# Kernel tuning notes

Measured on AMD Instinct MI355X. Metric: run time of the kernel, lower is better.

Reference implementation:

```python
import jax, jax.numpy as jnp
import numpy as np

WS = 8          # partition (window) size
HEADS = 8
DH = 32         # dim_head
DEPTH = 2
SCALE = DH ** -0.5
LN_EPS = 1e-5


def _rel_pos_index_dis(h, w):
    ch, cw = np.arange(h), np.arange(w)
    coords = np.stack(np.meshgrid(ch, cw, indexing='ij'))          # [2,h,w]
    cf = coords.reshape(2, -1)                                      # [2,n]
    rel = (cf[:, :, None] - cf[:, None, :]).transpose(1, 2, 0)      # [n,n,2]
    dis = (rel[:, :, 0].astype(np.float32) / h) ** 2 + (rel[:, :, 1].astype(np.float32) / w) ** 2
    rel = rel.copy()
    rel[:, :, 0] += h - 1
    rel[:, :, 1] += w - 1
    rel[:, :, 0] *= 2 * w - 1
    return rel.sum(-1), dis                                          # [n,n] int, [n,n] float


def _ln(x, g, b):
    m = x.mean(-1, keepdims=True)
    v = jnp.var(x, axis=-1, keepdims=True)
    return (x - m) * jax.lax.rsqrt(v + LN_EPS) * g + b


def setup_inputs() -> dict:
    key = jax.random.key(0)
    ks = jax.random.split(key, 16)
    D, INNER, MLP = 256, HEADS * DH, 1024
    TBL = (2 * WS - 1) * (2 * WS - 1)  # 225
    s = 0.02
    inp = {
        'x':        jax.random.normal(ks[0], (4, 256, 128, 128), jnp.float32),
        'W_patch':  jax.random.normal(ks[1], (256, D), jnp.float32) * s,
        'b_patch':  jnp.zeros((D,), jnp.float32),
        'ln1_g':    jnp.ones((DEPTH, D), jnp.float32),
        'ln1_b':    jnp.zeros((DEPTH, D), jnp.float32),
        'Wqkv':     jax.random.normal(ks[2], (DEPTH, D, 3 * INNER), jnp.float32) * s,
        'headsita': jnp.tile(jnp.arange(1, HEADS + 1, dtype=jnp.float32) * 0.1, (DEPTH, 1)),
        'bias_table': jax.random.normal(ks[3], (DEPTH, TBL, HEADS), jnp.float32) * s,
        'Wout':     jax.random.normal(ks[4], (DEPTH, INNER, D), jnp.float32) * s,
        'bout':     jnp.zeros((DEPTH, D), jnp.float32),
        'ln2_g':    jnp.ones((DEPTH, D), jnp.float32),
        'ln2_b':    jnp.zeros((DEPTH, D), jnp.float32),
        'W1':       jax.random.normal(ks[5], (DEPTH, D, MLP), jnp.float32) * s,
        'b1':       jnp.zeros((DEPTH, MLP), jnp.float32),
        'W2':       jax.random.normal(ks[6], (DEPTH, MLP, D), jnp.float32) * s,
        'b2':       jnp.zeros((DEPTH, D), jnp.float32),
    }
    return inp


def reference(x, W_patch, b_patch, ln1_g, ln1_b, Wqkv, headsita, bias_table,
              Wout, bout, ln2_g, ln2_b, W1, b1, W2, b2):
    B, C, H, W = x.shape
    n = WS * WS
    rpi_np, dis_np = _rel_pos_index_dis(WS, WS)
    rpi = jnp.asarray(rpi_np.reshape(-1))           # [n*n] int, static gather index
    dis = jnp.asarray(dis_np)                       # [n,n]

    # window partition: [B,C,H,W] -> [nW, n, C]
    t = x.transpose(0, 2, 3, 1)
    t = t.reshape(B, H // WS, WS, W // WS, WS, C).transpose(0, 1, 3, 2, 4, 5)
    t = t.reshape(-1, n, C)
    # patch embedding (patch_size=1)
    t = t @ W_patch + b_patch                        # [nW, n, D]

    attns = []
    for l in range(DEPTH):
        h = _ln(t, ln1_g[l], ln1_b[l])
        qkv = h @ Wqkv[l]                            # [nW, n, 3*inner]
        q, k, v = jnp.split(qkv, 3, axis=-1)
        def heads(a):
            return a.reshape(a.shape[0], n, HEADS, DH).transpose(0, 2, 1, 3)
        q, k, v = heads(q), heads(k), heads(v)       # [nW, H, n, dh]
        dots0 = jnp.einsum('bhid,bhjd->bhij', q, k) * SCALE
        # relative position bias gather: [n*n] -> [n,n,heads] -> [heads,n,n]
        bias = bias_table[l][rpi].reshape(n, n, HEADS).transpose(2, 0, 1)
        # learned per-head gaussian decay on spatial distance
        factor = 1.0 / (2.0 * headsita[l] ** 2 + 1e-10)          # [heads]
        pos = jnp.exp(-factor[:, None, None] * dis[None, :, :])  # [heads,n,n]
        dots = dots0 + bias[None] + 0.01 * pos[None]
        attn = jax.nn.softmax(dots, axis=-1)
        o = jnp.einsum('bhij,bhjd->bhid', attn, v)   # [nW, H, n, dh]
        o = o.transpose(0, 2, 1, 3).reshape(-1, n, HEADS * DH)
        ax = o @ Wout[l] + bout[l]
        attns.append(jax.nn.softmax(dots0, axis=-1))
        t = ax + t
        h2 = _ln(t, ln2_g[l], ln2_b[l])
        t = jax.nn.relu(h2 @ W1[l] + b1[l]) @ W2[l] + b2[l] + t

    # recover + window reverse: [nW, n, D] -> [B, D, H, W]
    D = t.shape[-1]
    out = t.reshape(B, H // WS, W // WS, WS, WS, D).transpose(0, 1, 3, 2, 4, 5)
    out = out.reshape(B, H, W, D).transpose(0, 3, 1, 2)
    return out, jnp.stack(attns)
```

## Files before the change

### kernel.cpp

```cpp
#include <hip/hip_runtime.h>
#include <hip/hip_bf16.h>
#include <cstddef>
#include <cstdint>


#define ROWS      65536
#define DMODEL    256
#define NWIN      1024
#define NHEADS    8
#define QKV_N     768
#define MLP_N     1024
#define SCALE_F   0.17677669529663687f
#define LN_EPS_F  1e-5f

typedef float f32x4 __attribute__((ext_vector_type(4)));
typedef __bf16 bf16x8 __attribute__((ext_vector_type(8)));

#define CP16(gp, lp)                                                          \
  __builtin_amdgcn_global_load_lds(                                           \
      (const __attribute__((address_space(1))) unsigned int*)(gp),            \
      (__attribute__((address_space(3))) unsigned int*)(lp), 16, 0, 0)

__device__ __forceinline__ float bf2f(ushort u) {
  return __uint_as_float(((unsigned)u) << 16);
}

__global__ __launch_bounds__(256) void gather_k(const float* __restrict__ x,
                                                __hip_bfloat16* __restrict__ Xg) {
  size_t idx = (size_t)blockIdx.x * 256 + threadIdx.x;
  int c   = (int)(idx & 255);
  int row = (int)(idx >> 8);
  int i   = row & 63;
  int wxy = row >> 6;
  int wx  = wxy & 15;
  int wy  = (wxy >> 4) & 15;
  int b   = wxy >> 8;
  int y   = wy * 8 + (i >> 3);
  int xx  = wx * 8 + (i & 7);
  Xg[idx] = __float2bfloat16(x[(((size_t)b * 256 + c) * 128 + y) * 128 + xx]);
}

__global__ __launch_bounds__(256) void unwindow_k(const float* __restrict__ t,
                                                  float* __restrict__ out) {
  size_t idx = (size_t)blockIdx.x * 256 + threadIdx.x;
  int xx = (int)(idx & 127);
  size_t r = idx >> 7;
  int y = (int)(r & 127); r >>= 7;
  int d = (int)(r & 255);
  int b = (int)(r >> 8);
  int row = ((b * 16 + (y >> 3)) * 16 + (xx >> 3)) * 64 + (y & 7) * 8 + (xx & 7);
  out[idx] = t[(size_t)row * DMODEL + d];
}

__global__ __launch_bounds__(256) void transpose_k(const float* __restrict__ src,
                                                   __hip_bfloat16* __restrict__ dst,
                                                   int K, int N) {
  __shared__ float tile[32][33];
  int tx = threadIdx.x, ty = threadIdx.y;
  int n0 = blockIdx.x * 32, k0 = blockIdx.y * 32;
#pragma unroll
  for (int i = 0; i < 4; ++i)
    tile[ty + i * 8][tx] = src[(size_t)(k0 + ty + i * 8) * N + n0 + tx];
  __syncthreads();
#pragma unroll
  for (int i = 0; i < 4; ++i)
    dst[(size_t)(n0 + ty + i * 8) * K + k0 + tx] =
        __float2bfloat16(tile[tx][ty + i * 8]);
}

__global__ __launch_bounds__(256) void ln_k(const float* __restrict__ X,
                                            __hip_bfloat16* __restrict__ Y,
                                            const float* __restrict__ g,
                                            const float* __restrict__ b) {
  const int row = blockIdx.x;
  const int tid = threadIdx.x;
  float x = X[(size_t)row * DMODEL + tid];
  float s = x, s2 = x * x;
#pragma unroll
  for (int off = 32; off > 0; off >>= 1) {
    s  += __shfl_down(s,  off);
    s2 += __shfl_down(s2, off);
  }
  __shared__ float ls[4], ls2[4];
  int wave = tid >> 6, lane = tid & 63;
  if (lane == 0) { ls[wave] = s; ls2[wave] = s2; }
  __syncthreads();
  if (tid == 0) {
    float ts  = ls[0] + ls[1] + ls[2] + ls[3];
    float ts2 = ls2[0] + ls2[1] + ls2[2] + ls2[3];
    float m   = ts * (1.0f / DMODEL);
    float var = ts2 * (1.0f / DMODEL) - m * m;
    ls[0]  = m;
    ls2[0] = rsqrtf(var + LN_EPS_F);
  }
  __syncthreads();
  float m = ls[0], rr = ls2[0];
  Y[(size_t)row * DMODEL + tid] = __float2bfloat16((x - m) * rr * g[tid] + b[tid]);
}

template <bool BIAS, bool RELU, bool RES, bool OBF16>
__global__ __launch_bounds__(256) void mm_k(const ushort* __restrict__ A,
                                            const ushort* __restrict__ BT,
                                            const float* __restrict__ bias,
                                            const float* __restrict__ res,
                                            void* __restrict__ Cout,
                                            int M, int N, int K) {
  __shared__ ushort As[4096];
  __shared__ ushort Bs[4096];
  const int tid = threadIdx.x;
  const int bm = blockIdx.y << 7, bn = blockIdx.x << 7;
  const ushort* Ap = A + (size_t)(bm + (tid >> 2)) * K + ((tid & 3) << 3);
  const ushort* Bp = BT + (size_t)(bn + (tid >> 2)) * K + ((tid & 3) << 3);
  const size_t k64 = (size_t)64 * K;
  const int lane = tid & 63, wave = tid >> 6;
  const int wm = (wave & 1) << 6, wn = (wave >> 1) << 6;
  const int lrow = lane & 15, kq = lane >> 4;
  const ushort* aF = &As[(wm + lrow) * 32 + kq * 8];
  const ushort* bF = &Bs[(wn + lrow) * 32 + kq * 8];
  f32x4 acc[4][4] = {};
  for (int k0 = 0; k0 < K; k0 += 32) {
    __syncthreads();
    CP16(Ap, &As[tid * 8]);
    CP16(Ap + k64, &As[2048 + tid * 8]);
    CP16(Bp, &Bs[tid * 8]);
    CP16(Bp + k64, &Bs[2048 + tid * 8]);
    Ap += 32; Bp += 32;
    __syncthreads();
    bf16x8 af[4], bf[4];
#pragma unroll
    for (int i = 0; i < 4; ++i) af[i] = *(const bf16x8*)(aF + i * 512);
#pragma unroll
    for (int j = 0; j < 4; ++j) bf[j] = *(const bf16x8*)(bF + j * 512);
#pragma unroll
    for (int i = 0; i < 4; ++i)
#pragma unroll
      for (int j = 0; j < 4; ++j)
        acc[i][j] =
            __builtin_amdgcn_mfma_f32_16x16x32_bf16(af[i], bf[j], acc[i][j], 0, 0, 0);
  }
  const int r0 = bm + wm + kq * 4;
  const int c0 = bn + wn + lrow;
#pragma unroll
  for (int i = 0; i < 4; ++i) {
#pragma unroll
    for (int j = 0; j < 4; ++j) {
      const int col = c0 + j * 16;
      const float bv = BIAS ? bias[col] : 0.f;
#pragma unroll
      for (int r = 0; r < 4; ++r) {
        const int row = r0 + i * 16 + r;
        float v = acc[i][j][r] + bv;
        if (RELU) v = fmaxf(v, 0.f);
        if (RES) v += res[(size_t)row * N + col];
        if (OBF16)
          ((__hip_bfloat16*)Cout)[(size_t)row * N + col] = __float2bfloat16(v);
        else
          ((float*)Cout)[(size_t)row * N + col] = v;
      }
    }
  }
}

__global__ __launch_bounds__(256) void attn_k(const ushort* __restrict__ qkv,
                                              __hip_bfloat16* __restrict__ o,
                                              float* __restrict__ attns_out,
                                              const float* __restrict__ bias_tbl,
                                              const float* __restrict__ sita_l) {
  const int w = blockIdx.x, head = blockIdx.y, tid = threadIdx.x;
  __shared__ float qs[64][36], ks[64][36], vs[64][36];
  __shared__ float s1[64][68];
  __shared__ float btbl[225];

  if (tid < 225) btbl[tid] = bias_tbl[tid * NHEADS + head];

  {
    const int i = tid >> 2, c = (tid & 3) * 8;
    const size_t rb = (size_t)(w * 64 + i) * QKV_N + head * 32 + c;
    union { uint4 u; ushort s[8]; } U;
    U.u = *(const uint4*)(qkv + rb);
#pragma unroll
    for (int z = 0; z < 8; ++z) qs[i][c + z] = bf2f(U.s[z]);
    U.u = *(const uint4*)(qkv + rb + 256);
#pragma unroll
    for (int z = 0; z < 8; ++z) ks[i][c + z] = bf2f(U.s[z]);
    U.u = *(const uint4*)(qkv + rb + 512);
#pragma unroll
    for (int z = 0; z < 8; ++z) vs[i][c + z] = bf2f(U.s[z]);
  }
  __syncthreads();

  const int i = tid >> 2, jq = tid & 3;
  const float sita = sita_l[head];
  const float factor = 1.0f / (2.0f * sita * sita + 1e-10f);
  const int iy = i >> 3, ix = i & 7;

  float ql[32];
#pragma unroll
  for (int c = 0; c < 8; ++c) *(float4*)&ql[c * 4] = *(const float4*)&qs[i][c * 4];

  float d0[16], e1[16];
#pragma unroll
  for (int jj = 0; jj < 16; ++jj) {
    const int j = jq * 16 + jj;
    float dot = 0.f;
#pragma unroll
    for (int cc = 0; cc < 8; ++cc) {
      const int c = (cc + jq * 2) & 7;
      const float4 kv = *(const float4*)&ks[j][c * 4];
      dot += ql[c * 4] * kv.x + ql[c * 4 + 1] * kv.y +
             ql[c * 4 + 2] * kv.z + ql[c * 4 + 3] * kv.w;
    }
    const float v0 = dot * SCALE_F;
    const int jy = j >> 3, jx = j & 7;
    const float dy = (float)(iy - jy) * 0.125f;
    const float dx = (float)(ix - jx) * 0.125f;
    const float bias = btbl[(iy - jy + 7) * 15 + (ix - jx + 7)];
    d0[jj] = v0;
    e1[jj] = v0 + bias + 0.01f * __expf(-factor * (dy * dy + dx * dx));
  }

  float m0 = -1e30f, m1 = -1e30f;
#pragma unroll
  for (int jj = 0; jj < 16; ++jj) {
    m0 = fmaxf(m0, d0[jj]);
    m1 = fmaxf(m1, e1[jj]);
  }
  m0 = fmaxf(m0, __shfl_xor(m0, 1)); m0 = fmaxf(m0, __shfl_xor(m0, 2));
  m1 = fmaxf(m1, __shfl_xor(m1, 1)); m1 = fmaxf(m1, __shfl_xor(m1, 2));
  float z0 = 0.f, z1 = 0.f;
#pragma unroll
  for (int jj = 0; jj < 16; ++jj) {
    d0[jj] = __expf(d0[jj] - m0); z0 += d0[jj];
    e1[jj] = __expf(e1[jj] - m1); z1 += e1[jj];
  }
  z0 += __shfl_xor(z0, 1); z0 += __shfl_xor(z0, 2);
  z1 += __shfl_xor(z1, 1); z1 += __shfl_xor(z1, 2);
  const float r0 = 1.f / z0, r1 = 1.f / z1;

  const size_t ab = (((size_t)(w * NHEADS + head)) * 64 + i) * 64 + jq * 16;
#pragma unroll
  for (int c4 = 0; c4 < 4; ++c4) {
    float4 t4 = make_float4(d0[c4 * 4] * r0, d0[c4 * 4 + 1] * r0,
                            d0[c4 * 4 + 2] * r0, d0[c4 * 4 + 3] * r0);
    *(float4*)(attns_out + ab + c4 * 4) = t4;
  }
#pragma unroll
  for (int jj = 0; jj < 16; ++jj) s1[i][jq * 16 + jj] = e1[jj] * r1;
  __syncthreads();

  const int dq = tid & 3;
  float acc[8] = {};
#pragma unroll
  for (int j = 0; j < 64; ++j) {
    const float a = s1[i][j];
    const float4 v0 = *(const float4*)&vs[j][dq * 8];
    const float4 v1 = *(const float4*)&vs[j][dq * 8 + 4];
    acc[0] += a * v0.x; acc[1] += a * v0.y; acc[2] += a * v0.z; acc[3] += a * v0.w;
    acc[4] += a * v1.x; acc[5] += a * v1.y; acc[6] += a * v1.z; acc[7] += a * v1.w;
  }
  union { uint4 u; __hip_bfloat16 b[8]; } O;
#pragma unroll
  for (int z = 0; z < 8; ++z) O.b[z] = __float2bfloat16(acc[z]);
  *(uint4*)((ushort*)o + (size_t)(w * 64 + i) * DMODEL + head * 32 + dq * 8) = O.u;
}

extern "C" void kernel_launch(void* const* d_in, const int* in_sizes, int n_in,
                              void* d_out, int out_size, void* d_ws, size_t ws_size,
                              hipStream_t stream) {
  const float* x        = (const float*)d_in[0];
  const float* W_patch  = (const float*)d_in[1];
  const float* b_patch  = (const float*)d_in[2];
  const float* ln1_g    = (const float*)d_in[3];
  const float* ln1_b    = (const float*)d_in[4];
  const float* Wqkv     = (const float*)d_in[5];
  const float* headsita = (const float*)d_in[6];
  const float* bias_tbl = (const float*)d_in[7];
  const float* Wout     = (const float*)d_in[8];
  const float* bout     = (const float*)d_in[9];
  const float* ln2_g    = (const float*)d_in[10];
  const float* ln2_b    = (const float*)d_in[11];
  const float* W1       = (const float*)d_in[12];
  const float* b1       = (const float*)d_in[13];
  const float* W2       = (const float*)d_in[14];
  const float* b2       = (const float*)d_in[15];

  char* W = (char*)d_ws;
  float*  t   = (float*)W;
  ushort* h   = (ushort*)(W + 67108864);
  ushort* qkv = (ushort*)(W + 100663296);
  ushort* o   = (ushort*)(W + 201326592);
  ushort* wT  = (ushort*)(W + 234881024);
  ushort* Xg  = qkv;
  ushort* hid = qkv;

  ushort* WpT   = wT;
  ushort* WqkvT = wT + 65536;
  ushort* WoutT = wT + 458752;
  ushort* W1T   = wT + 589824;
  ushort* W2T   = wT + 1114112;

  float* out_img = (float*)d_out;
  float* attns   = out_img + 16777216;

  const dim3 tb(32, 8);
  transpose_k<<<dim3(8, 8),  tb, 0, stream>>>(W_patch, (__hip_bfloat16*)WpT, 256, 256);
  for (int l = 0; l < 2; ++l) {
    transpose_k<<<dim3(24, 8), tb, 0, stream>>>(Wqkv + (size_t)l * 196608,
        (__hip_bfloat16*)(WqkvT + (size_t)l * 196608), 256, 768);
    transpose_k<<<dim3(8, 8),  tb, 0, stream>>>(Wout + (size_t)l * 65536,
        (__hip_bfloat16*)(WoutT + (size_t)l * 65536), 256, 256);
    transpose_k<<<dim3(32, 8), tb, 0, stream>>>(W1 + (size_t)l * 262144,
        (__hip_bfloat16*)(W1T + (size_t)l * 262144), 256, 1024);
    transpose_k<<<dim3(8, 32), tb, 0, stream>>>(W2 + (size_t)l * 262144,
        (__hip_bfloat16*)(W2T + (size_t)l * 262144), 1024, 256);
  }

  gather_k<<<65536, 256, 0, stream>>>(x, (__hip_bfloat16*)Xg);
  mm_k<true, false, false, false><<<dim3(2, 512), 256, 0, stream>>>(
      Xg, WpT, b_patch, nullptr, t, ROWS, DMODEL, DMODEL);

  for (int l = 0; l < 2; ++l) {
    ln_k<<<ROWS, 256, 0, stream>>>(t, (__hip_bfloat16*)h, ln1_g + l * 256, ln1_b + l * 256);
    mm_k<false, false, false, true><<<dim3(6, 512), 256, 0, stream>>>(
        h, WqkvT + (size_t)l * 196608, nullptr, nullptr, qkv, ROWS, QKV_N, DMODEL);
    attn_k<<<dim3(NWIN, NHEADS), 256, 0, stream>>>(
        qkv, (__hip_bfloat16*)o, attns + (size_t)l * 33554432,
        bias_tbl + l * 225 * NHEADS, headsita + l * NHEADS);
    mm_k<true, false, true, false><<<dim3(2, 512), 256, 0, stream>>>(
        o, WoutT + (size_t)l * 65536, bout + l * 256, t, t, ROWS, DMODEL, DMODEL);
    ln_k<<<ROWS, 256, 0, stream>>>(t, (__hip_bfloat16*)h, ln2_g + l * 256, ln2_b + l * 256);
    mm_k<true, true, false, true><<<dim3(8, 512), 256, 0, stream>>>(
        h, W1T + (size_t)l * 262144, b1 + l * MLP_N, nullptr, hid, ROWS, MLP_N, DMODEL);
    mm_k<true, false, true, false><<<dim3(2, 512), 256, 0, stream>>>(
        hid, W2T + (size_t)l * 262144, b2 + l * 256, t, t, ROWS, DMODEL, MLP_N);
  }

  unwindow_k<<<65536, 256, 0, stream>>>(t, out_img);
}
```

Measured before the change: 1.538 ms.

## Fuse LayerNorm into N=256 GEMM epilogues and move window attention onto MFMA

```diff
diff --git a/kernel.cpp b/kernel.cpp
--- a/kernel.cpp
+++ b/kernel.cpp
@@ -20,10 +20,6 @@
   __builtin_amdgcn_global_load_lds(                                           \
       (const __attribute__((address_space(1))) unsigned int*)(gp),            \
       (__attribute__((address_space(3))) unsigned int*)(lp), 16, 0, 0)
-
-__device__ __forceinline__ float bf2f(ushort u) {
-  return __uint_as_float(((unsigned)u) << 16);
-}
 
 __global__ __launch_bounds__(256) void gather_k(const float* __restrict__ x,
                                                 __hip_bfloat16* __restrict__ Xg) {
@@ -66,36 +62,6 @@
   for (int i = 0; i < 4; ++i)
     dst[(size_t)(n0 + ty + i * 8) * K + k0 + tx] =
         __float2bfloat16(tile[tx][ty + i * 8]);
-}
-
-__global__ __launch_bounds__(256) void ln_k(const float* __restrict__ X,
-                                            __hip_bfloat16* __restrict__ Y,
-                                            const float* __restrict__ g,
-                                            const float* __restrict__ b) {
-  const int row = blockIdx.x;
-  const int tid = threadIdx.x;
-  float x = X[(size_t)row * DMODEL + tid];
-  float s = x, s2 = x * x;
-#pragma unroll
-  for (int off = 32; off > 0; off >>= 1) {
-    s  += __shfl_down(s,  off);
-    s2 += __shfl_down(s2, off);
-  }
-  __shared__ float ls[4], ls2[4];
-  int wave = tid >> 6, lane = tid & 63;
-  if (lane == 0) { ls[wave] = s; ls2[wave] = s2; }
-  __syncthreads();
-  if (tid == 0) {
-    float ts  = ls[0] + ls[1] + ls[2] + ls[3];
-    float ts2 = ls2[0] + ls2[1] + ls2[2] + ls2[3];
-    float m   = ts * (1.0f / DMODEL);
-    float var = ts2 * (1.0f / DMODEL) - m * m;
-    ls[0]  = m;
-    ls2[0] = rsqrtf(var + LN_EPS_F);
-  }
-  __syncthreads();
-  float m = ls[0], rr = ls2[0];
-  Y[(size_t)row * DMODEL + tid] = __float2bfloat16((x - m) * rr * g[tid] + b[tid]);
 }
 
 template <bool BIAS, bool RELU, bool RES, bool OBF16>
@@ -161,107 +127,274 @@
   }
 }
 
+template <bool RES>
+__global__ __launch_bounds__(256) void mm_ln_k(const ushort* __restrict__ A,
+                                               const ushort* __restrict__ BT,
+                                               const float* __restrict__ bias,
+                                               const float* __restrict__ res,
+                                               float* __restrict__ Tout,
+                                               __hip_bfloat16* __restrict__ Hout,
+                                               const float* __restrict__ g,
+                                               const float* __restrict__ bb,
+                                               int K) {
+  __shared__ ushort As[2048];
+  __shared__ ushort Bs[8192];
+  __shared__ float rs[64][4], rs2[64][4];
+  const int tid = threadIdx.x;
+  const int bm = blockIdx.x << 6;
+  const ushort* Ap = A + (size_t)(bm + (tid >> 2)) * K + ((tid & 3) << 3);
+  const ushort* Bp = BT + (size_t)(tid >> 2) * K + ((tid & 3) << 3);
+  const size_t k64 = (size_t)64 * K;
+  const int lane = tid & 63, wave = tid >> 6;
+  const int l15 = lane & 15, quad = lane >> 4;
+  const ushort* aF = &As[l15 * 32 + quad * 8];
+  const ushort* bF = &Bs[(wave * 64 + l15) * 32 + quad * 8];
+  f32x4 acc[4][4] = {};
+  for (int k0 = 0; k0 < K; k0 += 32) {
+    __syncthreads();
+    CP16(Ap, &As[tid * 8]);
+    CP16(Bp, &Bs[tid * 8]);
+    CP16(Bp + k64, &Bs[2048 + tid * 8]);
+    CP16(Bp + 2 * k64, &Bs[4096 + tid * 8]);
+    CP16(Bp + 3 * k64, &Bs[6144 + tid * 8]);
+    Ap += 32; Bp += 32;
+    __syncthreads();
+    bf16x8 af[4], bf[4];
+#pragma unroll
+    for (int i = 0; i < 4; ++i) af[i] = *(const bf16x8*)(aF + i * 512);
+#pragma unroll
+    for (int j = 0; j < 4; ++j) bf[j] = *(const bf16x8*)(bF + j * 512);
+#pragma unroll
+    for (int i = 0; i < 4; ++i)
+#pragma unroll
+      for (int j = 0; j < 4; ++j)
+        acc[i][j] =
+            __builtin_amdgcn_mfma_f32_16x16x32_bf16(af[i], bf[j], acc[i][j], 0, 0, 0);
+  }
+  const int rb = quad * 4;
+#pragma unroll
+  for (int i = 0; i < 4; ++i)
+#pragma unroll
+    for (int j = 0; j < 4; ++j) {
+      const int col = wave * 64 + j * 16 + l15;
+      const float bv = bias[col];
+#pragma unroll
+      for (int r = 0; r < 4; ++r) {
+        const int row = bm + i * 16 + rb + r;
+        float x = acc[i][j][r] + bv;
+        if (RES) x += res[(size_t)row * 256 + col];
+        acc[i][j][r] = x;
+      }
+    }
+#pragma unroll
+  for (int i = 0; i < 4; ++i)
+#pragma unroll
+    for (int r = 0; r < 4; ++r) {
+      float s = 0.f, s2 = 0.f;
+#pragma unroll
+      for (int j = 0; j < 4; ++j) {
+        float x = acc[i][j][r];
+        s += x; s2 += x * x;
+      }
+      s += __shfl_xor(s, 1);  s += __shfl_xor(s, 2);
+      s += __shfl_xor(s, 4);  s += __shfl_xor(s, 8);
+      s2 += __shfl_xor(s2, 1); s2 += __shfl_xor(s2, 2);
+      s2 += __shfl_xor(s2, 4); s2 += __shfl_xor(s2, 8);
+      if (l15 == 0) {
+        rs[i * 16 + rb + r][wave] = s;
+        rs2[i * 16 + rb + r][wave] = s2;
+      }
+    }
+  __syncthreads();
+  float mrow[4][4], rrow[4][4];
+#pragma unroll
+  for (int i = 0; i < 4; ++i)
+#pragma unroll
+    for (int r = 0; r < 4; ++r) {
+      const int lr = i * 16 + rb + r;
+      float4 s4 = *(const float4*)rs[lr];
+      float4 q4 = *(const float4*)rs2[lr];
+      float tot = s4.x + s4.y + s4.z + s4.w;
+      float tot2 = q4.x + q4.y + q4.z + q4.w;
+      float m = tot * (1.0f / 256.0f);
+      float var = tot2 * (1.0f / 256.0f) - m * m;
+      mrow[i][r] = m;
+      rrow[i][r] = rsqrtf(var + LN_EPS_F);
+    }
+#pragma unroll
+  for (int i = 0; i < 4; ++i)
+#pragma unroll
+    for (int j = 0; j < 4; ++j) {
+      const int col = wave * 64 + j * 16 + l15;
+      const float gv = g[col], bv = bb[col];
+#pragma unroll
+      for (int r = 0; r < 4; ++r) {
+        const int row = bm + i * 16 + rb + r;
+        float x = acc[i][j][r];
+        Tout[(size_t)row * 256 + col] = x;
+        Hout[(size_t)row * 256 + col] =
+            __float2bfloat16((x - mrow[i][r]) * rrow[i][r] * gv + bv);
+      }
+    }
+}
+
 __global__ __launch_bounds__(256) void attn_k(const ushort* __restrict__ qkv,
                                               __hip_bfloat16* __restrict__ o,
                                               float* __restrict__ attns_out,
                                               const float* __restrict__ bias_tbl,
                                               const float* __restrict__ sita_l) {
-  const int w = blockIdx.x, head = blockIdx.y, tid = threadIdx.x;
-  __shared__ float qs[64][36], ks[64][36], vs[64][36];
-  __shared__ float s1[64][68];
-  __shared__ float btbl[225];
-
-  if (tid < 225) btbl[tid] = bias_tbl[tid * NHEADS + head];
-
-  {
-    const int i = tid >> 2, c = (tid & 3) * 8;
-    const size_t rb = (size_t)(w * 64 + i) * QKV_N + head * 32 + c;
-    union { uint4 u; ushort s[8]; } U;
-    U.u = *(const uint4*)(qkv + rb);
-#pragma unroll
-    for (int z = 0; z < 8; ++z) qs[i][c + z] = bf2f(U.s[z]);
-    U.u = *(const uint4*)(qkv + rb + 256);
-#pragma unroll
-    for (int z = 0; z < 8; ++z) ks[i][c + z] = bf2f(U.s[z]);
-    U.u = *(const uint4*)(qkv + rb + 512);
-#pragma unroll
-    for (int z = 0; z < 8; ++z) vs[i][c + z] = bf2f(U.s[z]);
-  }
-  __syncthreads();
-
-  const int i = tid >> 2, jq = tid & 3;
+  __shared__ ushort smem[4 * 7424];
+  __shared__ float tbl[225];
+  const int tid = threadIdx.x;
+  const int lane = tid & 63, wave = tid >> 6;
+  const int head = blockIdx.x & 7;
+  const int w = ((blockIdx.x >> 3) << 2) + wave;
+  ushort* qw = smem + wave * 7424;
+  ushort* kw = qw + 2560;
+  ushort* vw = kw + 2560;
+  ushort* Pw = qw;
+
   const float sita = sita_l[head];
   const float factor = 1.0f / (2.0f * sita * sita + 1e-10f);
-  const int iy = i >> 3, ix = i & 7;
-
-  float ql[32];
-#pragma unroll
-  for (int c = 0; c < 8; ++c) *(float4*)&ql[c * 4] = *(const float4*)&qs[i][c * 4];
-
-  float d0[16], e1[16];
-#pragma unroll
-  for (int jj = 0; jj < 16; ++jj) {
-    const int j = jq * 16 + jj;
-    float dot = 0.f;
-#pragma unroll
-    for (int cc = 0; cc < 8; ++cc) {
-      const int c = (cc + jq * 2) & 7;
-      const float4 kv = *(const float4*)&ks[j][c * 4];
-      dot += ql[c * 4] * kv.x + ql[c * 4 + 1] * kv.y +
-             ql[c * 4 + 2] * kv.z + ql[c * 4 + 3] * kv.w;
-    }
-    const float v0 = dot * SCALE_F;
-    const int jy = j >> 3, jx = j & 7;
-    const float dy = (float)(iy - jy) * 0.125f;
-    const float dx = (float)(ix - jx) * 0.125f;
-    const float bias = btbl[(iy - jy + 7) * 15 + (ix - jx + 7)];
-    d0[jj] = v0;
-    e1[jj] = v0 + bias + 0.01f * __expf(-factor * (dy * dy + dx * dx));
-  }
-
-  float m0 = -1e30f, m1 = -1e30f;
-#pragma unroll
-  for (int jj = 0; jj < 16; ++jj) {
-    m0 = fmaxf(m0, d0[jj]);
-    m1 = fmaxf(m1, e1[jj]);
-  }
-  m0 = fmaxf(m0, __shfl_xor(m0, 1)); m0 = fmaxf(m0, __shfl_xor(m0, 2));
-  m1 = fmaxf(m1, __shfl_xor(m1, 1)); m1 = fmaxf(m1, __shfl_xor(m1, 2));
-  float z0 = 0.f, z1 = 0.f;
-#pragma unroll
-  for (int jj = 0; jj < 16; ++jj) {
-    d0[jj] = __expf(d0[jj] - m0); z0 += d0[jj];
-    e1[jj] = __expf(e1[jj] - m1); z1 += e1[jj];
-  }
-  z0 += __shfl_xor(z0, 1); z0 += __shfl_xor(z0, 2);
-  z1 += __shfl_xor(z1, 1); z1 += __shfl_xor(z1, 2);
-  const float r0 = 1.f / z0, r1 = 1.f / z1;
-
-  const size_t ab = (((size_t)(w * NHEADS + head)) * 64 + i) * 64 + jq * 16;
-#pragma unroll
-  for (int c4 = 0; c4 < 4; ++c4) {
-    float4 t4 = make_float4(d0[c4 * 4] * r0, d0[c4 * 4 + 1] * r0,
-                            d0[c4 * 4 + 2] * r0, d0[c4 * 4 + 3] * r0);
-    *(float4*)(attns_out + ab + c4 * 4) = t4;
-  }
-#pragma unroll
-  for (int jj = 0; jj < 16; ++jj) s1[i][jq * 16 + jj] = e1[jj] * r1;
+  for (int idx = tid; idx < 225; idx += 256) {
+    int dyi = idx / 15 - 7, dxi = idx % 15 - 7;
+    float dis = (float)(dyi * dyi + dxi * dxi) * 0.015625f;
+    tbl[idx] = bias_tbl[idx * NHEADS + head] + 0.01f * __expf(-factor * dis);
+  }
+
+  {
+    const ushort* base = qkv + (size_t)(w * 64) * QKV_N + head * 32;
+    const int r0 = lane >> 2, c = (lane & 3) << 3;
+#pragma unroll
+    for (int r4 = 0; r4 < 4; ++r4) {
+      const int row = r4 * 16 + r0;
+      const ushort* rp = base + (size_t)row * QKV_N + c;
+      *(uint4*)(qw + row * 40 + c) = *(const uint4*)(rp);
+      *(uint4*)(kw + row * 40 + c) = *(const uint4*)(rp + 256);
+      union { uint4 u; ushort s[8]; } V;
+      V.u = *(const uint4*)(rp + 512);
+#pragma unroll
+      for (int z = 0; z < 8; ++z) vw[(c + z) * 72 + row] = V.s[z];
+    }
+  }
   __syncthreads();
 
-  const int dq = tid & 3;
-  float acc[8] = {};
-#pragma unroll
-  for (int j = 0; j < 64; ++j) {
-    const float a = s1[i][j];
-    const float4 v0 = *(const float4*)&vs[j][dq * 8];
-    const float4 v1 = *(const float4*)&vs[j][dq * 8 + 4];
-    acc[0] += a * v0.x; acc[1] += a * v0.y; acc[2] += a * v0.z; acc[3] += a * v0.w;
-    acc[4] += a * v1.x; acc[5] += a * v1.y; acc[6] += a * v1.z; acc[7] += a * v1.w;
-  }
-  union { uint4 u; __hip_bfloat16 b[8]; } O;
-#pragma unroll
-  for (int z = 0; z < 8; ++z) O.b[z] = __float2bfloat16(acc[z]);
-  *(uint4*)((ushort*)o + (size_t)(w * 64 + i) * DMODEL + head * 32 + dq * 8) = O.u;
+  const int l15 = lane & 15, quad = lane >> 4;
+
+  f32x4 acc[4][4] = {};
+  {
+    bf16x8 af[4], bfr[4];
+#pragma unroll
+    for (int i = 0; i < 4; ++i)
+      af[i] = *(const bf16x8*)(qw + (i * 16 + l15) * 40 + quad * 8);
+#pragma unroll
+    for (int j = 0; j < 4; ++j)
+      bfr[j] = *(const bf16x8*)(kw + (j * 16 + l15) * 40 + quad * 8);
+#pragma unroll
+    for (int i = 0; i < 4; ++i)
+#pragma unroll
+      for (int j = 0; j < 4; ++j)
+        acc[i][j] =
+            __builtin_amdgcn_mfma_f32_16x16x32_bf16(af[i], bfr[j], acc[i][j], 0, 0, 0);
+  }
+
+  float e1[4][4][4];
+#pragma unroll
+  for (int i = 0; i < 4; ++i)
+#pragma unroll
+    for (int r = 0; r < 4; ++r) {
+      const int row = i * 16 + quad * 4 + r;
+      const int iy = row >> 3, ix = row & 7;
+#pragma unroll
+      for (int j = 0; j < 4; ++j) {
+        const int col = j * 16 + l15;
+        const int jy = col >> 3, jx = col & 7;
+        float d0 = acc[i][j][r] * SCALE_F;
+        acc[i][j][r] = d0;
+        e1[i][j][r] = d0 + tbl[(iy - jy + 7) * 15 + (ix - jx + 7)];
+      }
+    }
+
+#pragma unroll
+  for (int i = 0; i < 4; ++i)
+#pragma unroll
+    for (int r = 0; r < 4; ++r) {
+      float m0 = -1e30f, m1 = -1e30f;
+#pragma unroll
+      for (int j = 0; j < 4; ++j) {
+        m0 = fmaxf(m0, acc[i][j][r]);
+        m1 = fmaxf(m1, e1[i][j][r]);
+      }
+      m0 = fmaxf(m0, __shfl_xor(m0, 1)); m0 = fmaxf(m0, __shfl_xor(m0, 2));
+      m0 = fmaxf(m0, __shfl_xor(m0, 4)); m0 = fmaxf(m0, __shfl_xor(m0, 8));
+      m1 = fmaxf(m1, __shfl_xor(m1, 1)); m1 = fmaxf(m1, __shfl_xor(m1, 2));
+      m1 = fmaxf(m1, __shfl_xor(m1, 4)); m1 = fmaxf(m1, __shfl_xor(m1, 8));
+      float z0 = 0.f, z1 = 0.f;
+#pragma unroll
+      for (int j = 0; j < 4; ++j) {
+        float a = __expf(acc[i][j][r] - m0); acc[i][j][r] = a; z0 += a;
+        float bqq = __expf(e1[i][j][r] - m1); e1[i][j][r] = bqq; z1 += bqq;
+      }
+      z0 += __shfl_xor(z0, 1); z0 += __shfl_xor(z0, 2);
+      z0 += __shfl_xor(z0, 4); z0 += __shfl_xor(z0, 8);
+      z1 += __shfl_xor(z1, 1); z1 += __shfl_xor(z1, 2);
+      z1 += __shfl_xor(z1, 4); z1 += __shfl_xor(z1, 8);
+      const float r0i = 1.f / z0, r1i = 1.f / z1;
+#pragma unroll
+      for (int j = 0; j < 4; ++j) {
+        acc[i][j][r] *= r0i;
+        e1[i][j][r] *= r1i;
+      }
+    }
+
+  {
+    float* ab = attns_out + ((size_t)(w * NHEADS + head)) * 4096;
+#pragma unroll
+    for (int i = 0; i < 4; ++i)
+#pragma unroll
+      for (int j = 0; j < 4; ++j)
+#pragma unroll
+        for (int r = 0; r < 4; ++r)
+          ab[(i * 16 + quad * 4 + r) * 64 + j * 16 + l15] = acc[i][j][r];
+  }
+
+#pragma unroll
+  for (int i = 0; i < 4; ++i)
+#pragma unroll
+    for (int j = 0; j < 4; ++j)
+#pragma unroll
+      for (int r = 0; r < 4; ++r)
+        Pw[(i * 16 + quad * 4 + r) * 72 + j * 16 + l15] =
+            ((__hip_bfloat16_raw)__float2bfloat16(e1[i][j][r])).x;
+
+  f32x4 oacc[4][2] = {};
+#pragma unroll
+  for (int ks = 0; ks < 2; ++ks) {
+    bf16x8 pa[4], vb[2];
+#pragma unroll
+    for (int i = 0; i < 4; ++i)
+      pa[i] = *(const bf16x8*)(Pw + (i * 16 + l15) * 72 + ks * 32 + quad * 8);
+#pragma unroll
+    for (int j = 0; j < 2; ++j)
+      vb[j] = *(const bf16x8*)(vw + (j * 16 + l15) * 72 + ks * 32 + quad * 8);
+#pragma unroll
+    for (int i = 0; i < 4; ++i)
+#pragma unroll
+      for (int j = 0; j < 2; ++j)
+        oacc[i][j] =
+            __builtin_amdgcn_mfma_f32_16x16x32_bf16(pa[i], vb[j], oacc[i][j], 0, 0, 0);
+  }
+  {
+    ushort* ob = (ushort*)o + (size_t)(w * 64) * DMODEL + head * 32;
+#pragma unroll
+    for (int i = 0; i < 4; ++i)
+#pragma unroll
+      for (int j = 0; j < 2; ++j)
+#pragma unroll
+        for (int r = 0; r < 4; ++r)
+          ob[(size_t)(i * 16 + quad * 4 + r) * DMODEL + j * 16 + l15] =
+              ((__hip_bfloat16_raw)__float2bfloat16(oacc[i][j][r])).x;
+  }
 }
 
 extern "C" void kernel_launch(void* const* d_in, const int* in_sizes, int n_in,
@@ -316,23 +449,27 @@
   }
 
   gather_k<<<65536, 256, 0, stream>>>(x, (__hip_bfloat16*)Xg);
-  mm_k<true, false, false, false><<<dim3(2, 512), 256, 0, stream>>>(
-      Xg, WpT, b_patch, nullptr, t, ROWS, DMODEL, DMODEL);
+  mm_ln_k<false><<<1024, 256, 0, stream>>>(
+      Xg, WpT, b_patch, nullptr, t, (__hip_bfloat16*)h, ln1_g, ln1_b, 256);
 
   for (int l = 0; l < 2; ++l) {
-    ln_k<<<ROWS, 256, 0, stream>>>(t, (__hip_bfloat16*)h, ln1_g + l * 256, ln1_b + l * 256);
     mm_k<false, false, false, true><<<dim3(6, 512), 256, 0, stream>>>(
         h, WqkvT + (size_t)l * 196608, nullptr, nullptr, qkv, ROWS, QKV_N, DMODEL);
-    attn_k<<<dim3(NWIN, NHEADS), 256, 0, stream>>>(
+    attn_k<<<2048, 256, 0, stream>>>(
         qkv, (__hip_bfloat16*)o, attns + (size_t)l * 33554432,
         bias_tbl + l * 225 * NHEADS, headsita + l * NHEADS);
-    mm_k<true, false, true, false><<<dim3(2, 512), 256, 0, stream>>>(
-        o, WoutT + (size_t)l * 65536, bout + l * 256, t, t, ROWS, DMODEL, DMODEL);
-    ln_k<<<ROWS, 256, 0, stream>>>(t, (__hip_bfloat16*)h, ln2_g + l * 256, ln2_b + l * 256);
+    mm_ln_k<true><<<1024, 256, 0, stream>>>(
+        o, WoutT + (size_t)l * 65536, bout + l * 256, t, t, (__hip_bfloat16*)h,
+        ln2_g + l * 256, ln2_b + l * 256, 256);
     mm_k<true, true, false, true><<<dim3(8, 512), 256, 0, stream>>>(
         h, W1T + (size_t)l * 262144, b1 + l * MLP_N, nullptr, hid, ROWS, MLP_N, DMODEL);
-    mm_k<true, false, true, false><<<dim3(2, 512), 256, 0, stream>>>(
-        hid, W2T + (size_t)l * 262144, b2 + l * 256, t, t, ROWS, DMODEL, MLP_N);
+    if (l == 0) {
+      mm_ln_k<true><<<1024, 256, 0, stream>>>(
+          hid, W2T, b2, t, t, (__hip_bfloat16*)h, ln1_g + 256, ln1_b + 256, 1024);
+    } else {
+      mm_k<true, false, true, false><<<dim3(2, 512), 256, 0, stream>>>(
+          hid, W2T + 262144, b2 + 256, t, t, ROWS, DMODEL, MLP_N);
+    }
   }
 
   unwindow_k<<<65536, 256, 0, stream>>>(t, out_img);
```

Measured after the change: 1.372 ms. -10.8%, faster.
